# Kernel tuning notes

Hardware: AMD Instinct MI355X
Metric: run time of the kernel (lower is better)

The kernel has to match this reference:

```python
import jax, jax.numpy as jnp
import numpy as np

D_MODEL = 1024
NUM_HEADS = 16
KEY_DIM = 64
VALUE_DIM = 64
NEG_INF = jnp.float32(-1e30)


def setup_inputs() -> dict:
    key = jax.random.key(0)
    ks = jax.random.split(key, 10)
    B, S = 2, 2048
    lim = 1.0 / np.sqrt(D_MODEL)
    x = jax.random.normal(ks[0], (B, S, D_MODEL), dtype=jnp.float32)
    mask = jnp.ones((B, S), dtype=jnp.int32)  # pad mask: 1 = keep
    # stacked per-head linear params (Linear stores weight as [out, in])
    Wq = jax.random.uniform(ks[1], (NUM_HEADS, KEY_DIM, D_MODEL), jnp.float32, -lim, lim)
    bq = jax.random.uniform(ks[2], (NUM_HEADS, KEY_DIM), jnp.float32, -lim, lim)
    Wk = jax.random.uniform(ks[3], (NUM_HEADS, KEY_DIM, D_MODEL), jnp.float32, -lim, lim)
    bk = jax.random.uniform(ks[4], (NUM_HEADS, KEY_DIM), jnp.float32, -lim, lim)
    Wv = jax.random.uniform(ks[5], (NUM_HEADS, VALUE_DIM, D_MODEL), jnp.float32, -lim, lim)
    bv = jax.random.uniform(ks[6], (NUM_HEADS, VALUE_DIM), jnp.float32, -lim, lim)
    lim_o = 1.0 / np.sqrt(NUM_HEADS * VALUE_DIM)
    Wo = jax.random.uniform(ks[7], (D_MODEL, NUM_HEADS * VALUE_DIM), jnp.float32, -lim_o, lim_o)
    bo = jax.random.uniform(ks[8], (D_MODEL,), jnp.float32, -lim_o, lim_o)
    return {"x": x, "mask": mask, "Wq": Wq, "bq": bq, "Wk": Wk, "bk": bk,
            "Wv": Wv, "bv": bv, "Wo": Wo, "bo": bo}


def _mha(x, mask, Wq, bq, Wk, bk, Wv, bv, Wo, bo):
    B, S, _ = x.shape
    # per-head projections: [B, H, S, k]
    q = jnp.einsum('bsd,hkd->bhsk', x, Wq) + bq[None, :, None, :]
    k = jnp.einsum('bsd,hkd->bhsk', x, Wk) + bk[None, :, None, :]
    v = jnp.einsum('bsd,hvd->bhsv', x, Wv) + bv[None, :, None, :]
    scale = 1.0 / np.sqrt(KEY_DIM).astype(np.float32)
    scores = jnp.einsum('bhik,bhjk->bhij', q, k) * scale  # [B, H, S, S]
    # final mask = causal AND pad-row AND pad-col
    causal = jnp.tril(jnp.ones((S, S), dtype=bool))
    pad = mask.astype(bool)
    final = causal[None, None] & pad[:, None, :, None] & pad[:, None, None, :]
    masked = jnp.where(final, scores, NEG_INF)
    w = jax.nn.softmax(masked, axis=-1)
    w = jnp.where(final, w, 0.0)  # fully-masked rows -> zeros, matching loop impl
    out = jnp.einsum('bhij,bhjv->bhiv', w, v)            # [B, H, S, V]
    concat = out.transpose(0, 2, 1, 3).reshape(B, S, NUM_HEADS * VALUE_DIM)
    return concat @ Wo.T + bo


def reference(x, mask, Wq, bq, Wk, bk, Wv, bv, Wo, bo):
    return _mha(x, mask, Wq, bq, Wk, bk, Wv, bv, Wo, bo)
```

## Files before the change

kernel.cpp:

```cpp
#include <hip/hip_runtime.h>

#define SEQ 2048
#define NH 16
#define HD 64
#define DMODEL 1024

__device__ __forceinline__ unsigned int f2bf(float f) {
  unsigned int u = __float_as_uint(f);
  return ((u + 0x7fffu + ((u >> 16) & 1u)) >> 16) & 0xffffu;
}

typedef __bf16 bf16x8 __attribute__((ext_vector_type(8)));
typedef float f32x4 __attribute__((ext_vector_type(4)));

__device__ __forceinline__ void gl2lds16(const unsigned short* g, unsigned short* l) {
  __builtin_amdgcn_global_load_lds(
      (const __attribute__((address_space(1))) unsigned int*)g,
      (__attribute__((address_space(3))) unsigned int*)l, 16, 0, 0);
}

__global__ __launch_bounds__(256) void cast_all_kernel(
    const float* __restrict__ x, const float* __restrict__ wq,
    const float* __restrict__ wk, const float* __restrict__ wv,
    const float* __restrict__ wo,
    unsigned short* __restrict__ xb, unsigned short* __restrict__ wqb,
    unsigned short* __restrict__ wkb, unsigned short* __restrict__ wvb,
    unsigned short* __restrict__ wob) {
  int idx = blockIdx.x * 256 + threadIdx.x;
  if (idx >= 1048576) return;
  const float* src;
  unsigned short* dst;
  int off;
  if (idx < 524288) {
    src = x; dst = xb; off = idx;
  } else {
    int t = idx - 524288;
    int w = t >> 17;
    off = t & 131071;
    src = (w == 0) ? wq : (w == 1) ? wk : (w == 2) ? wv : wo;
    dst = (w == 0) ? wqb : (w == 1) ? wkb : (w == 2) ? wvb : wob;
  }
  const float4* p = reinterpret_cast<const float4*>(src) + (size_t)off * 2;
  float4 a = p[0], b = p[1];
  uint4 o;
  o.x = f2bf(a.x) | (f2bf(a.y) << 16);
  o.y = f2bf(a.z) | (f2bf(a.w) << 16);
  o.z = f2bf(b.x) | (f2bf(b.y) << 16);
  o.w = f2bf(b.z) | (f2bf(b.w) << 16);
  reinterpret_cast<uint4*>(dst)[off] = o;
}

template <int MODE>
__global__ __launch_bounds__(256) void gemm128(
    const unsigned short* __restrict__ A, const unsigned short* __restrict__ B,
    const float* __restrict__ bias0, const float* __restrict__ bias1,
    const float* __restrict__ bias2, float* __restrict__ Cf,
    unsigned short* __restrict__ Qo, unsigned short* __restrict__ Ko,
    unsigned short* __restrict__ Vto, int Kdim) {
  __shared__ __align__(16) unsigned short As[128 * 64];
  __shared__ __align__(16) unsigned short Bs[128 * 64];
  const int tid = threadIdx.x;
  const int wave = tid >> 6, lane = tid & 63;
  const int wm = wave >> 1, wn = wave & 1;
  const int fr = lane & 15, quad = lane >> 4;
  const int fx = fr & 7;
  const int n0 = blockIdx.x * 128, m0 = blockIdx.y * 128;

  const int srowg = lane >> 3;
  const int schunk = (lane & 7) ^ (srowg & 7);
  const unsigned short* Abase =
      A + (size_t)(m0 + wave * 32 + srowg) * Kdim + schunk * 8;
  const unsigned short* Bbase =
      B + (size_t)(n0 + wave * 32 + srowg) * Kdim + schunk * 8;
  unsigned short* AsW = As + (wave * 32) * 64;
  unsigned short* BsW = Bs + (wave * 32) * 64;

  f32x4 acc[4][4];
#pragma unroll
  for (int mt = 0; mt < 4; ++mt)
#pragma unroll
    for (int nt = 0; nt < 4; ++nt) acc[mt][nt] = f32x4{0.f, 0.f, 0.f, 0.f};

  for (int k0 = 0; k0 < Kdim; k0 += 64) {
#pragma unroll
    for (int t = 0; t < 4; ++t) {
      gl2lds16(Abase + (size_t)(t * 8) * Kdim + k0, AsW + t * 8 * 64);
      gl2lds16(Bbase + (size_t)(t * 8) * Kdim + k0, BsW + t * 8 * 64);
    }
    __syncthreads();
#pragma unroll
    for (int ks = 0; ks < 2; ++ks) {
      bf16x8 af[4], bfv[4];
#pragma unroll
      for (int mt = 0; mt < 4; ++mt)
        af[mt] = *reinterpret_cast<const bf16x8*>(
            As + (wm * 64 + mt * 16 + fr) * 64 + ((ks * 4 + quad) ^ fx) * 8);
#pragma unroll
      for (int nt = 0; nt < 4; ++nt)
        bfv[nt] = *reinterpret_cast<const bf16x8*>(
            Bs + (wn * 64 + nt * 16 + fr) * 64 + ((ks * 4 + quad) ^ fx) * 8);
#pragma unroll
      for (int mt = 0; mt < 4; ++mt)
#pragma unroll
        for (int nt = 0; nt < 4; ++nt)
          acc[mt][nt] = __builtin_amdgcn_mfma_f32_16x16x32_bf16(
              af[mt], bfv[nt], acc[mt][nt], 0, 0, 0);
    }
    __syncthreads();
  }

  if (MODE == 0) {
    const int seg = n0 >> 10;
    const float* bp = (seg == 0) ? bias0 : (seg == 1) ? bias1 : bias2;
    const float scale = (seg == 0) ? 0.125f : 1.0f;
    unsigned short* QK = (seg == 0) ? Qo : Ko;
#pragma unroll
    for (int nt = 0; nt < 4; ++nt) {
      const int c = (n0 + wn * 64 + nt * 16 + fr) & 1023;
      const int h = c >> 6, d = c & 63;
      const float bs = bp[c];
#pragma unroll
      for (int mt = 0; mt < 4; ++mt) {
        const int mbase = m0 + wm * 64 + mt * 16 + quad * 4;
        const int b = mbase >> 11, s0 = mbase & 2047;
        if (seg < 2) {
          unsigned short* dst = QK + (((size_t)(b * NH + h)) * SEQ + s0) * HD + d;
#pragma unroll
          for (int r = 0; r < 4; ++r)
            dst[(size_t)r * HD] = (unsigned short)f2bf((acc[mt][nt][r] + bs) * scale);
        } else {
          ushort4 pk;
          pk.x = (unsigned short)f2bf(acc[mt][nt][0] + bs);
          pk.y = (unsigned short)f2bf(acc[mt][nt][1] + bs);
          pk.z = (unsigned short)f2bf(acc[mt][nt][2] + bs);
          pk.w = (unsigned short)f2bf(acc[mt][nt][3] + bs);
          *reinterpret_cast<ushort4*>(
              Vto + (((size_t)(b * NH + h)) * HD + d) * SEQ + s0) = pk;
        }
      }
    }
  } else {
#pragma unroll
    for (int nt = 0; nt < 4; ++nt) {
      const int cg = n0 + wn * 64 + nt * 16 + fr;
      const float bs = bias0[cg];
#pragma unroll
      for (int mt = 0; mt < 4; ++mt) {
        const int mbase = m0 + wm * 64 + mt * 16 + quad * 4;
#pragma unroll
        for (int r = 0; r < 4; ++r)
          Cf[(size_t)(mbase + r) * DMODEL + cg] = acc[mt][nt][r] + bs;
      }
    }
  }
}

__global__ __launch_bounds__(256) void attn_mfma_kernel(const unsigned short* __restrict__ Qg,
                                                        const unsigned short* __restrict__ Kg,
                                                        const unsigned short* __restrict__ Vtg,
                                                        const int* __restrict__ mask,
                                                        unsigned short* __restrict__ concat) {
  const int group = blockIdx.x >> 5;
  const int ib = (group < 8) ? (15 - group) : (group - 8);
  const int bh = blockIdx.x & 31;
  const int b = bh >> 4;
  const int h = bh & 15;
  const int tid = threadIdx.x;
  const int wave = tid >> 6;
  const int lane = tid & 63;
  const int quad = lane >> 4;
  const int fr = lane & 15;
  const int i0 = ib * 128;

  __shared__ unsigned short Ks[64][72];
  __shared__ unsigned short Vts[64][72];
  __shared__ unsigned short Pt[4][16][72];

  const unsigned short* Qb = Qg + ((size_t)bh * SEQ) * HD;
  const unsigned short* Kb = Kg + ((size_t)bh * SEQ) * HD;
  const unsigned short* Vtb = Vtg + ((size_t)bh * HD) * SEQ;
  const int* maskb = mask + b * SEQ;

  int irow[2];
  bf16x8 qf[2][2];
  int padi[2];
#pragma unroll
  for (int qc = 0; qc < 2; ++qc) {
    irow[qc] = i0 + qc * 64 + wave * 16 + fr;
    qf[qc][0] = *reinterpret_cast<const bf16x8*>(Qb + (size_t)irow[qc] * HD + quad * 8);
    qf[qc][1] = *reinterpret_cast<const bf16x8*>(Qb + (size_t)irow[qc] * HD + quad * 8 + 32);
    padi[qc] = maskb[irow[qc]];
  }

  f32x4 o[2][4];
#pragma unroll
  for (int qc = 0; qc < 2; ++qc)
#pragma unroll
    for (int vt = 0; vt < 4; ++vt) o[qc][vt] = f32x4{0.f, 0.f, 0.f, 0.f};
  float mrun[2] = {-1e30f, -1e30f}, lrun[2] = {0.f, 0.f};

  const int srow = tid >> 2;
  const int spart = (tid & 3) * 2;
  const int njc = 2 * ib + 2;

  for (int jc = 0; jc < njc; ++jc) {
    const int j0 = jc * 64;
    {
      const uint4* kg = reinterpret_cast<const uint4*>(Kb + (size_t)(j0 + srow) * HD);
      const uint4* vg = reinterpret_cast<const uint4*>(Vtb + (size_t)srow * SEQ + j0);
      uint4 ka = kg[spart], kc = kg[spart + 1];
      uint4 va = vg[spart], vc = vg[spart + 1];
      *reinterpret_cast<uint4*>(&Ks[srow][spart * 8]) = ka;
      *reinterpret_cast<uint4*>(&Ks[srow][spart * 8 + 8]) = kc;
      *reinterpret_cast<uint4*>(&Vts[srow][spart * 8]) = va;
      *reinterpret_cast<uint4*>(&Vts[srow][spart * 8 + 8]) = vc;
    }
    __syncthreads();

    const int4* mp = reinterpret_cast<const int4*>(maskb + j0);
    int4 mvv[4];
#pragma unroll
    for (int jt = 0; jt < 4; ++jt) mvv[jt] = mp[jt * 4 + quad];

#pragma unroll
    for (int qc = 0; qc < 2; ++qc) {
      if (qc == 0 && jc == 2 * ib + 1) continue;
      const bool diag = (jc == 2 * ib + qc);
      const int ir = irow[qc];

      f32x4 st[4];
#pragma unroll
      for (int jt = 0; jt < 4; ++jt) {
        st[jt] = f32x4{0.f, 0.f, 0.f, 0.f};
        bf16x8 ka0 = *reinterpret_cast<const bf16x8*>(&Ks[jt * 16 + fr][quad * 8]);
        bf16x8 ka1 = *reinterpret_cast<const bf16x8*>(&Ks[jt * 16 + fr][quad * 8 + 32]);
        st[jt] = __builtin_amdgcn_mfma_f32_16x16x32_bf16(ka0, qf[qc][0], st[jt], 0, 0, 0);
        st[jt] = __builtin_amdgcn_mfma_f32_16x16x32_bf16(ka1, qf[qc][1], st[jt], 0, 0, 0);
      }

#pragma unroll
      for (int jt = 0; jt < 4; ++jt) {
        const int4 mv = mvv[jt];
        const int jb = j0 + jt * 16 + quad * 4;
        if (mv.x == 0 || (diag && jb + 0 > ir)) st[jt][0] = -1e30f;
        if (mv.y == 0 || (diag && jb + 1 > ir)) st[jt][1] = -1e30f;
        if (mv.z == 0 || (diag && jb + 2 > ir)) st[jt][2] = -1e30f;
        if (mv.w == 0 || (diag && jb + 3 > ir)) st[jt][3] = -1e30f;
      }

      float tmax = -1e30f;
#pragma unroll
      for (int jt = 0; jt < 4; ++jt)
#pragma unroll
        for (int r = 0; r < 4; ++r) tmax = fmaxf(tmax, st[jt][r]);
      tmax = fmaxf(tmax, __shfl_xor(tmax, 16));
      tmax = fmaxf(tmax, __shfl_xor(tmax, 32));
      float mnew = fmaxf(fmaxf(mrun[qc], tmax), -1e20f);
      const float corr = __expf(mrun[qc] - mnew);
      float p[16];
      float lloc = 0.f;
#pragma unroll
      for (int jt = 0; jt < 4; ++jt)
#pragma unroll
        for (int r = 0; r < 4; ++r) {
          float pv = __expf(st[jt][r] - mnew);
          p[jt * 4 + r] = pv;
          lloc += pv;
        }
      lloc += __shfl_xor(lloc, 16);
      lloc += __shfl_xor(lloc, 32);
      lrun[qc] = lrun[qc] * corr + lloc;
      mrun[qc] = mnew;

#pragma unroll
      for (int jt = 0; jt < 4; ++jt) {
        ushort4 pk;
        pk.x = (unsigned short)f2bf(p[jt * 4 + 0]);
        pk.y = (unsigned short)f2bf(p[jt * 4 + 1]);
        pk.z = (unsigned short)f2bf(p[jt * 4 + 2]);
        pk.w = (unsigned short)f2bf(p[jt * 4 + 3]);
        *reinterpret_cast<ushort4*>(&Pt[wave][fr][jt * 16 + quad * 4]) = pk;
      }

#pragma unroll
      for (int vt = 0; vt < 4; ++vt) {
        o[qc][vt][0] *= corr; o[qc][vt][1] *= corr;
        o[qc][vt][2] *= corr; o[qc][vt][3] *= corr;
      }

      bf16x8 pa0 = *reinterpret_cast<const bf16x8*>(&Pt[wave][fr][quad * 8]);
      bf16x8 pa1 = *reinterpret_cast<const bf16x8*>(&Pt[wave][fr][quad * 8 + 32]);
#pragma unroll
      for (int vt = 0; vt < 4; ++vt) {
        bf16x8 vb0 = *reinterpret_cast<const bf16x8*>(&Vts[vt * 16 + fr][quad * 8]);
        bf16x8 vb1 = *reinterpret_cast<const bf16x8*>(&Vts[vt * 16 + fr][quad * 8 + 32]);
        o[qc][vt] = __builtin_amdgcn_mfma_f32_16x16x32_bf16(vb0, pa0, o[qc][vt], 0, 0, 0);
        o[qc][vt] = __builtin_amdgcn_mfma_f32_16x16x32_bf16(vb1, pa1, o[qc][vt], 0, 0, 0);
      }
    }
    __syncthreads();
  }

#pragma unroll
  for (int qc = 0; qc < 2; ++qc) {
    const float inv = (padi[qc] != 0 && lrun[qc] > 0.f) ? 1.f / lrun[qc] : 0.f;
    unsigned short* orow = concat + ((size_t)(b * SEQ + irow[qc])) * DMODEL + h * HD;
#pragma unroll
    for (int vt = 0; vt < 4; ++vt) {
      ushort4 pk;
      pk.x = (unsigned short)f2bf(o[qc][vt][0] * inv);
      pk.y = (unsigned short)f2bf(o[qc][vt][1] * inv);
      pk.z = (unsigned short)f2bf(o[qc][vt][2] * inv);
      pk.w = (unsigned short)f2bf(o[qc][vt][3] * inv);
      *reinterpret_cast<ushort4*>(orow + vt * 16 + quad * 4) = pk;
    }
  }
}

extern "C" void kernel_launch(void* const* d_in, const int* in_sizes, int n_in,
                              void* d_out, int out_size, void* d_ws, size_t ws_size,
                              hipStream_t stream) {
  (void)in_sizes; (void)n_in; (void)out_size;
  const float* x  = (const float*)d_in[0];
  const int* mask = (const int*)d_in[1];
  const float* Wq = (const float*)d_in[2];
  const float* bq = (const float*)d_in[3];
  const float* Wk = (const float*)d_in[4];
  const float* bk = (const float*)d_in[5];
  const float* Wv = (const float*)d_in[6];
  const float* bv = (const float*)d_in[7];
  const float* Wo = (const float*)d_in[8];
  const float* bo = (const float*)d_in[9];
  float* out = (float*)d_out;

  char* ws = (char*)d_ws;
  if (ws_size < (48ull << 20)) return;
  unsigned short* xb  = (unsigned short*)(ws);
  unsigned short* wqb = (unsigned short*)(ws + (8ull  << 20));
  unsigned short* wkb = (unsigned short*)(ws + (10ull << 20));
  unsigned short* wvb = (unsigned short*)(ws + (12ull << 20));
  unsigned short* wob = (unsigned short*)(ws + (14ull << 20));
  unsigned short* Qb  = (unsigned short*)(ws + (16ull << 20));
  unsigned short* Kb  = (unsigned short*)(ws + (24ull << 20));
  unsigned short* Vtb = (unsigned short*)(ws + (32ull << 20));
  unsigned short* cb  = (unsigned short*)(ws + (40ull << 20));

  cast_all_kernel<<<4096, 256, 0, stream>>>(x, Wq, Wk, Wv, Wo, xb, wqb, wkb, wvb, wob);

  gemm128<0><<<dim3(24, 32), 256, 0, stream>>>(xb, wqb, bq, bk, bv,
                                               nullptr, Qb, Kb, Vtb, 1024);

  attn_mfma_kernel<<<512, 256, 0, stream>>>(Qb, Kb, Vtb, mask, cb);

  gemm128<1><<<dim3(8, 32), 256, 0, stream>>>(cb, wob, bo, nullptr, nullptr,
                                              out, nullptr, nullptr, nullptr, 1024);
}
```

Before: 214.6 us.

## Pair mirrored query tiles per block, skip mask checks on all-valid tiles, use exp2

```diff
diff --git a/kernel.cpp b/kernel.cpp
--- a/kernel.cpp
+++ b/kernel.cpp
@@ -8,6 +8,12 @@
 __device__ __forceinline__ unsigned int f2bf(float f) {
   unsigned int u = __float_as_uint(f);
   return ((u + 0x7fffu + ((u >> 16) & 1u)) >> 16) & 0xffffu;
+}
+
+__device__ __forceinline__ unsigned int pk2bf(float a, float b) {
+  unsigned short ua = __builtin_bit_cast(unsigned short, (__bf16)a);
+  unsigned short ub = __builtin_bit_cast(unsigned short, (__bf16)b);
+  return (unsigned int)ua | ((unsigned int)ub << 16);
 }
 
 typedef __bf16 bf16x8 __attribute__((ext_vector_type(8)));
@@ -47,7 +53,7 @@
   o.y = f2bf(a.z) | (f2bf(a.w) << 16);
   o.z = f2bf(b.x) | (f2bf(b.y) << 16);
   o.w = f2bf(b.z) | (f2bf(b.w) << 16);
-  reinterpret_cast<uint4*>(dst)[off] = o;
+  reinterpret_cast<uint4*>(dst)[idx == off ? off : off] = o;
 }
 
 template <int MODE>
@@ -112,7 +118,7 @@
   if (MODE == 0) {
     const int seg = n0 >> 10;
     const float* bp = (seg == 0) ? bias0 : (seg == 1) ? bias1 : bias2;
-    const float scale = (seg == 0) ? 0.125f : 1.0f;
+    const float scale = (seg == 0) ? 0.1803368809f : 1.0f;
     unsigned short* QK = (seg == 0) ? Qo : Ko;
 #pragma unroll
     for (int nt = 0; nt < 4; ++nt) {
@@ -129,12 +135,10 @@
           for (int r = 0; r < 4; ++r)
             dst[(size_t)r * HD] = (unsigned short)f2bf((acc[mt][nt][r] + bs) * scale);
         } else {
-          ushort4 pk;
-          pk.x = (unsigned short)f2bf(acc[mt][nt][0] + bs);
-          pk.y = (unsigned short)f2bf(acc[mt][nt][1] + bs);
-          pk.z = (unsigned short)f2bf(acc[mt][nt][2] + bs);
-          pk.w = (unsigned short)f2bf(acc[mt][nt][3] + bs);
-          *reinterpret_cast<ushort4*>(
+          uint2 pk;
+          pk.x = pk2bf(acc[mt][nt][0] + bs, acc[mt][nt][1] + bs);
+          pk.y = pk2bf(acc[mt][nt][2] + bs, acc[mt][nt][3] + bs);
+          *reinterpret_cast<uint2*>(
               Vto + (((size_t)(b * NH + h)) * HD + d) * SEQ + s0) = pk;
         }
       }
@@ -155,13 +159,11 @@
   }
 }
 
-__global__ __launch_bounds__(256) void attn_mfma_kernel(const unsigned short* __restrict__ Qg,
-                                                        const unsigned short* __restrict__ Kg,
-                                                        const unsigned short* __restrict__ Vtg,
-                                                        const int* __restrict__ mask,
-                                                        unsigned short* __restrict__ concat) {
-  const int group = blockIdx.x >> 5;
-  const int ib = (group < 8) ? (15 - group) : (group - 8);
+__global__ __launch_bounds__(256, 3) void attn_mfma_kernel(
+    const unsigned short* __restrict__ Qg, const unsigned short* __restrict__ Kg,
+    const unsigned short* __restrict__ Vtg, const int* __restrict__ mask,
+    unsigned short* __restrict__ concat) {
+  const int g = blockIdx.x >> 5;
   const int bh = blockIdx.x & 31;
   const int b = bh >> 4;
   const int h = bh & 15;
@@ -170,40 +172,46 @@
   const int lane = tid & 63;
   const int quad = lane >> 4;
   const int fr = lane & 15;
-  const int i0 = ib * 128;
+  const int ibA = 31 - g, ibB = g;
 
   __shared__ unsigned short Ks[64][72];
   __shared__ unsigned short Vts[64][72];
-  __shared__ unsigned short Pt[4][16][72];
+  __shared__ unsigned short Pt[2][4][16][72];
+  __shared__ unsigned int tilebad;
 
   const unsigned short* Qb = Qg + ((size_t)bh * SEQ) * HD;
   const unsigned short* Kb = Kg + ((size_t)bh * SEQ) * HD;
   const unsigned short* Vtb = Vtg + ((size_t)bh * HD) * SEQ;
   const int* maskb = mask + b * SEQ;
 
-  int irow[2];
-  bf16x8 qf[2][2];
-  int padi[2];
-#pragma unroll
-  for (int qc = 0; qc < 2; ++qc) {
-    irow[qc] = i0 + qc * 64 + wave * 16 + fr;
-    qf[qc][0] = *reinterpret_cast<const bf16x8*>(Qb + (size_t)irow[qc] * HD + quad * 8);
-    qf[qc][1] = *reinterpret_cast<const bf16x8*>(Qb + (size_t)irow[qc] * HD + quad * 8 + 32);
-    padi[qc] = maskb[irow[qc]];
-  }
-
-  f32x4 o[2][4];
-#pragma unroll
-  for (int qc = 0; qc < 2; ++qc)
-#pragma unroll
-    for (int vt = 0; vt < 4; ++vt) o[qc][vt] = f32x4{0.f, 0.f, 0.f, 0.f};
-  float mrun[2] = {-1e30f, -1e30f}, lrun[2] = {0.f, 0.f};
+  if (tid == 0) tilebad = 0;
+  __syncthreads();
+  {
+    const int4* mp4 = reinterpret_cast<const int4*>(maskb);
+    int4 a = mp4[tid * 2], c = mp4[tid * 2 + 1];
+    if (!(a.x && a.y && a.z && a.w && c.x && c.y && c.z && c.w))
+      atomicOr(&tilebad, 1u << (tid >> 3));
+  }
+  __syncthreads();
+  const unsigned int tbad = tilebad;
+
+  const int irA = ibA * 64 + wave * 16 + fr;
+  const int irB = ibB * 64 + wave * 16 + fr;
+  const bf16x8 qA0 = *reinterpret_cast<const bf16x8*>(Qb + (size_t)irA * HD + quad * 8);
+  const bf16x8 qA1 = *reinterpret_cast<const bf16x8*>(Qb + (size_t)irA * HD + quad * 8 + 32);
+  const bf16x8 qB0 = *reinterpret_cast<const bf16x8*>(Qb + (size_t)irB * HD + quad * 8);
+  const bf16x8 qB1 = *reinterpret_cast<const bf16x8*>(Qb + (size_t)irB * HD + quad * 8 + 32);
+  const int padA = maskb[irA], padB = maskb[irB];
+
+  f32x4 oA[4], oB[4];
+#pragma unroll
+  for (int vt = 0; vt < 4; ++vt) { oA[vt] = f32x4{0,0,0,0}; oB[vt] = f32x4{0,0,0,0}; }
+  float mA = -1e20f, lA = 0.f, mB = -1e20f, lB = 0.f;
 
   const int srow = tid >> 2;
   const int spart = (tid & 3) * 2;
-  const int njc = 2 * ib + 2;
-
-  for (int jc = 0; jc < njc; ++jc) {
+
+  for (int jc = 0; jc <= ibA; ++jc) {
     const int j0 = jc * 64;
     {
       const uint4* kg = reinterpret_cast<const uint4*>(Kb + (size_t)(j0 + srow) * HD);
@@ -217,102 +225,161 @@
     }
     __syncthreads();
 
-    const int4* mp = reinterpret_cast<const int4*>(maskb + j0);
-    int4 mvv[4];
-#pragma unroll
-    for (int jt = 0; jt < 4; ++jt) mvv[jt] = mp[jt * 4 + quad];
-
-#pragma unroll
-    for (int qc = 0; qc < 2; ++qc) {
-      if (qc == 0 && jc == 2 * ib + 1) continue;
-      const bool diag = (jc == 2 * ib + qc);
-      const int ir = irow[qc];
-
-      f32x4 st[4];
+    const bool doB = (jc <= ibB);
+    const bool diagA = (jc == ibA), diagB = (jc == ibB);
+    const bool tb = (tbad >> jc) & 1u;
+
+    f32x4 stA[4], stB[4];
+#pragma unroll
+    for (int jt = 0; jt < 4; ++jt) {
+      bf16x8 ka0 = *reinterpret_cast<const bf16x8*>(&Ks[jt * 16 + fr][quad * 8]);
+      bf16x8 ka1 = *reinterpret_cast<const bf16x8*>(&Ks[jt * 16 + fr][quad * 8 + 32]);
+      stA[jt] = f32x4{0,0,0,0};
+      stA[jt] = __builtin_amdgcn_mfma_f32_16x16x32_bf16(ka0, qA0, stA[jt], 0, 0, 0);
+      stA[jt] = __builtin_amdgcn_mfma_f32_16x16x32_bf16(ka1, qA1, stA[jt], 0, 0, 0);
+      if (doB) {
+        stB[jt] = f32x4{0,0,0,0};
+        stB[jt] = __builtin_amdgcn_mfma_f32_16x16x32_bf16(ka0, qB0, stB[jt], 0, 0, 0);
+        stB[jt] = __builtin_amdgcn_mfma_f32_16x16x32_bf16(ka1, qB1, stB[jt], 0, 0, 0);
+      }
+    }
+
+    if (tb) {
+      const int4* mp = reinterpret_cast<const int4*>(maskb + j0);
 #pragma unroll
       for (int jt = 0; jt < 4; ++jt) {
-        st[jt] = f32x4{0.f, 0.f, 0.f, 0.f};
-        bf16x8 ka0 = *reinterpret_cast<const bf16x8*>(&Ks[jt * 16 + fr][quad * 8]);
-        bf16x8 ka1 = *reinterpret_cast<const bf16x8*>(&Ks[jt * 16 + fr][quad * 8 + 32]);
-        st[jt] = __builtin_amdgcn_mfma_f32_16x16x32_bf16(ka0, qf[qc][0], st[jt], 0, 0, 0);
-        st[jt] = __builtin_amdgcn_mfma_f32_16x16x32_bf16(ka1, qf[qc][1], st[jt], 0, 0, 0);
-      }
-
+        const int4 mv = mp[jt * 4 + quad];
+        if (mv.x == 0) { stA[jt][0] = -1e30f; if (doB) stB[jt][0] = -1e30f; }
+        if (mv.y == 0) { stA[jt][1] = -1e30f; if (doB) stB[jt][1] = -1e30f; }
+        if (mv.z == 0) { stA[jt][2] = -1e30f; if (doB) stB[jt][2] = -1e30f; }
+        if (mv.w == 0) { stA[jt][3] = -1e30f; if (doB) stB[jt][3] = -1e30f; }
+      }
+    }
+    if (diagA) {
 #pragma unroll
       for (int jt = 0; jt < 4; ++jt) {
-        const int4 mv = mvv[jt];
         const int jb = j0 + jt * 16 + quad * 4;
-        if (mv.x == 0 || (diag && jb + 0 > ir)) st[jt][0] = -1e30f;
-        if (mv.y == 0 || (diag && jb + 1 > ir)) st[jt][1] = -1e30f;
-        if (mv.z == 0 || (diag && jb + 2 > ir)) st[jt][2] = -1e30f;
-        if (mv.w == 0 || (diag && jb + 3 > ir)) st[jt][3] = -1e30f;
-      }
-
+#pragma unroll
+        for (int r = 0; r < 4; ++r)
+          if (jb + r > irA) stA[jt][r] = -1e30f;
+      }
+    }
+    if (doB && diagB) {
+#pragma unroll
+      for (int jt = 0; jt < 4; ++jt) {
+        const int jb = j0 + jt * 16 + quad * 4;
+#pragma unroll
+        for (int r = 0; r < 4; ++r)
+          if (jb + r > irB) stB[jt][r] = -1e30f;
+      }
+    }
+
+    {
       float tmax = -1e30f;
 #pragma unroll
       for (int jt = 0; jt < 4; ++jt)
 #pragma unroll
-        for (int r = 0; r < 4; ++r) tmax = fmaxf(tmax, st[jt][r]);
+        for (int r = 0; r < 4; ++r) tmax = fmaxf(tmax, stA[jt][r]);
       tmax = fmaxf(tmax, __shfl_xor(tmax, 16));
       tmax = fmaxf(tmax, __shfl_xor(tmax, 32));
-      float mnew = fmaxf(fmaxf(mrun[qc], tmax), -1e20f);
-      const float corr = __expf(mrun[qc] - mnew);
-      float p[16];
+      const bool upd = __ballot(tmax > mA) != 0ull;
+      float corr = 1.f;
+      if (upd) { const float mn = fmaxf(mA, tmax); corr = __builtin_amdgcn_exp2f(mA - mn); mA = mn; }
       float lloc = 0.f;
 #pragma unroll
-      for (int jt = 0; jt < 4; ++jt)
-#pragma unroll
-        for (int r = 0; r < 4; ++r) {
-          float pv = __expf(st[jt][r] - mnew);
-          p[jt * 4 + r] = pv;
-          lloc += pv;
-        }
+      for (int jt = 0; jt < 4; ++jt) {
+        float p0 = __builtin_amdgcn_exp2f(stA[jt][0] - mA);
+        float p1 = __builtin_amdgcn_exp2f(stA[jt][1] - mA);
+        float p2 = __builtin_amdgcn_exp2f(stA[jt][2] - mA);
+        float p3 = __builtin_amdgcn_exp2f(stA[jt][3] - mA);
+        lloc += (p0 + p1) + (p2 + p3);
+        uint2 pk; pk.x = pk2bf(p0, p1); pk.y = pk2bf(p2, p3);
+        *reinterpret_cast<uint2*>(&Pt[0][wave][fr][jt * 16 + quad * 4]) = pk;
+      }
       lloc += __shfl_xor(lloc, 16);
       lloc += __shfl_xor(lloc, 32);
-      lrun[qc] = lrun[qc] * corr + lloc;
-      mrun[qc] = mnew;
-
+      if (upd) {
+        lA = lA * corr + lloc;
+#pragma unroll
+        for (int vt = 0; vt < 4; ++vt) {
+          oA[vt][0] *= corr; oA[vt][1] *= corr; oA[vt][2] *= corr; oA[vt][3] *= corr;
+        }
+      } else lA += lloc;
+    }
+    if (doB) {
+      float tmax = -1e30f;
+#pragma unroll
+      for (int jt = 0; jt < 4; ++jt)
+#pragma unroll
+        for (int r = 0; r < 4; ++r) tmax = fmaxf(tmax, stB[jt][r]);
+      tmax = fmaxf(tmax, __shfl_xor(tmax, 16));
+      tmax = fmaxf(tmax, __shfl_xor(tmax, 32));
+      const bool upd = __ballot(tmax > mB) != 0ull;
+      float corr = 1.f;
+      if (upd) { const float mn = fmaxf(mB, tmax); corr = __builtin_amdgcn_exp2f(mB - mn); mB = mn; }
+      float lloc = 0.f;
 #pragma unroll
       for (int jt = 0; jt < 4; ++jt) {
-        ushort4 pk;
-        pk.x = (unsigned short)f2bf(p[jt * 4 + 0]);
-        pk.y = (unsigned short)f2bf(p[jt * 4 + 1]);
-        pk.z = (unsigned short)f2bf(p[jt * 4 + 2]);
-        pk.w = (unsigned short)f2bf(p[jt * 4 + 3]);
-        *reinterpret_cast<ushort4*>(&Pt[wave][fr][jt * 16 + quad * 4]) = pk;
-      }
-
-#pragma unroll
-      for (int vt = 0; vt < 4; ++vt) {
-        o[qc][vt][0] *= corr; o[qc][vt][1] *= corr;
-        o[qc][vt][2] *= corr; o[qc][vt][3] *= corr;
-      }
-
-      bf16x8 pa0 = *reinterpret_cast<const bf16x8*>(&Pt[wave][fr][quad * 8]);
-      bf16x8 pa1 = *reinterpret_cast<const bf16x8*>(&Pt[wave][fr][quad * 8 + 32]);
-#pragma unroll
-      for (int vt = 0; vt < 4; ++vt) {
-        bf16x8 vb0 = *reinterpret_cast<const bf16x8*>(&Vts[vt * 16 + fr][quad * 8]);
-        bf16x8 vb1 = *reinterpret_cast<const bf16x8*>(&Vts[vt * 16 + fr][quad * 8 + 32]);
-        o[qc][vt] = __builtin_amdgcn_mfma_f32_16x16x32_bf16(vb0, pa0, o[qc][vt], 0, 0, 0);
-        o[qc][vt] = __builtin_amdgcn_mfma_f32_16x16x32_bf16(vb1, pa1, o[qc][vt], 0, 0, 0);
+        float p0 = __builtin_amdgcn_exp2f(stB[jt][0] - mB);
+        float p1 = __builtin_amdgcn_exp2f(stB[jt][1] - mB);
+        float p2 = __builtin_amdgcn_exp2f(stB[jt][2] - mB);
+        float p3 = __builtin_amdgcn_exp2f(stB[jt][3] - mB);
+        lloc += (p0 + p1) + (p2 + p3);
+        uint2 pk; pk.x = pk2bf(p0, p1); pk.y = pk2bf(p2, p3);
+        *reinterpret_cast<uint2*>(&Pt[1][wave][fr][jt * 16 + quad * 4]) = pk;
+      }
+      lloc += __shfl_xor(lloc, 16);
+      lloc += __shfl_xor(lloc, 32);
+      if (upd) {
+        lB = lB * corr + lloc;
+#pragma unroll
+        for (int vt = 0; vt < 4; ++vt) {
+          oB[vt][0] *= corr; oB[vt][1] *= corr; oB[vt][2] *= corr; oB[vt][3] *= corr;
+        }
+      } else lB += lloc;
+    }
+
+    bf16x8 paA0 = *reinterpret_cast<const bf16x8*>(&Pt[0][wave][fr][quad * 8]);
+    bf16x8 paA1 = *reinterpret_cast<const bf16x8*>(&Pt[0][wave][fr][quad * 8 + 32]);
+    bf16x8 paB0, paB1;
+    if (doB) {
+      paB0 = *reinterpret_cast<const bf16x8*>(&Pt[1][wave][fr][quad * 8]);
+      paB1 = *reinterpret_cast<const bf16x8*>(&Pt[1][wave][fr][quad * 8 + 32]);
+    }
+#pragma unroll
+    for (int vt = 0; vt < 4; ++vt) {
+      bf16x8 vb0 = *reinterpret_cast<const bf16x8*>(&Vts[vt * 16 + fr][quad * 8]);
+      bf16x8 vb1 = *reinterpret_cast<const bf16x8*>(&Vts[vt * 16 + fr][quad * 8 + 32]);
+      oA[vt] = __builtin_amdgcn_mfma_f32_16x16x32_bf16(vb0, paA0, oA[vt], 0, 0, 0);
+      oA[vt] = __builtin_amdgcn_mfma_f32_16x16x32_bf16(vb1, paA1, oA[vt], 0, 0, 0);
+      if (doB) {
+        oB[vt] = __builtin_amdgcn_mfma_f32_16x16x32_bf16(vb0, paB0, oB[vt], 0, 0, 0);
+        oB[vt] = __builtin_amdgcn_mfma_f32_16x16x32_bf16(vb1, paB1, oB[vt], 0, 0, 0);
       }
     }
     __syncthreads();
   }
 
-#pragma unroll
-  for (int qc = 0; qc < 2; ++qc) {
-    const float inv = (padi[qc] != 0 && lrun[qc] > 0.f) ? 1.f / lrun[qc] : 0.f;
-    unsigned short* orow = concat + ((size_t)(b * SEQ + irow[qc])) * DMODEL + h * HD;
+  {
+    const float inv = (padA != 0 && lA > 0.f) ? 1.f / lA : 0.f;
+    unsigned short* orow = concat + ((size_t)(b * SEQ + irA)) * DMODEL + h * HD;
 #pragma unroll
     for (int vt = 0; vt < 4; ++vt) {
-      ushort4 pk;
-      pk.x = (unsigned short)f2bf(o[qc][vt][0] * inv);
-      pk.y = (unsigned short)f2bf(o[qc][vt][1] * inv);
-      pk.z = (unsigned short)f2bf(o[qc][vt][2] * inv);
-      pk.w = (unsigned short)f2bf(o[qc][vt][3] * inv);
-      *reinterpret_cast<ushort4*>(orow + vt * 16 + quad * 4) = pk;
+      uint2 pk;
+      pk.x = pk2bf(oA[vt][0] * inv, oA[vt][1] * inv);
+      pk.y = pk2bf(oA[vt][2] * inv, oA[vt][3] * inv);
+      *reinterpret_cast<uint2*>(orow + vt * 16 + quad * 4) = pk;
+    }
+  }
+  {
+    const float inv = (padB != 0 && lB > 0.f) ? 1.f / lB : 0.f;
+    unsigned short* orow = concat + ((size_t)(b * SEQ + irB)) * DMODEL + h * HD;
+#pragma unroll
+    for (int vt = 0; vt < 4; ++vt) {
+      uint2 pk;
+      pk.x = pk2bf(oB[vt][0] * inv, oB[vt][1] * inv);
+      pk.y = pk2bf(oB[vt][2] * inv, oB[vt][3] * inv);
+      *reinterpret_cast<uint2*>(orow + vt * 16 + quad * 4) = pk;
     }
   }
 }
```

Result: faster. 200.6 us (-6.5%).

## Restructure attention: 4 balanced query tiles per block, K/V in registers, exp2 softmax

Applied to the files above, without the earlier changes.

```diff
diff --git a/kernel.cpp b/kernel.cpp
--- a/kernel.cpp
+++ b/kernel.cpp
@@ -8,6 +8,12 @@
 __device__ __forceinline__ unsigned int f2bf(float f) {
   unsigned int u = __float_as_uint(f);
   return ((u + 0x7fffu + ((u >> 16) & 1u)) >> 16) & 0xffffu;
+}
+
+__device__ __forceinline__ unsigned int pk2bf(float a, float b) {
+  unsigned short ua = __builtin_bit_cast(unsigned short, (__bf16)a);
+  unsigned short ub = __builtin_bit_cast(unsigned short, (__bf16)b);
+  return (unsigned int)ua | ((unsigned int)ub << 16);
 }
 
 typedef __bf16 bf16x8 __attribute__((ext_vector_type(8)));
@@ -112,7 +118,7 @@
   if (MODE == 0) {
     const int seg = n0 >> 10;
     const float* bp = (seg == 0) ? bias0 : (seg == 1) ? bias1 : bias2;
-    const float scale = (seg == 0) ? 0.125f : 1.0f;
+    const float scale = (seg == 0) ? 0.1803368809f : 1.0f;
     unsigned short* QK = (seg == 0) ? Qo : Ko;
 #pragma unroll
     for (int nt = 0; nt < 4; ++nt) {
@@ -129,12 +135,10 @@
           for (int r = 0; r < 4; ++r)
             dst[(size_t)r * HD] = (unsigned short)f2bf((acc[mt][nt][r] + bs) * scale);
         } else {
-          ushort4 pk;
-          pk.x = (unsigned short)f2bf(acc[mt][nt][0] + bs);
-          pk.y = (unsigned short)f2bf(acc[mt][nt][1] + bs);
-          pk.z = (unsigned short)f2bf(acc[mt][nt][2] + bs);
-          pk.w = (unsigned short)f2bf(acc[mt][nt][3] + bs);
-          *reinterpret_cast<ushort4*>(
+          uint2 pk;
+          pk.x = pk2bf(acc[mt][nt][0] + bs, acc[mt][nt][1] + bs);
+          pk.y = pk2bf(acc[mt][nt][2] + bs, acc[mt][nt][3] + bs);
+          *reinterpret_cast<uint2*>(
               Vto + (((size_t)(b * NH + h)) * HD + d) * SEQ + s0) = pk;
         }
       }
@@ -155,97 +159,101 @@
   }
 }
 
-__global__ __launch_bounds__(256) void attn_mfma_kernel(const unsigned short* __restrict__ Qg,
-                                                        const unsigned short* __restrict__ Kg,
-                                                        const unsigned short* __restrict__ Vtg,
-                                                        const int* __restrict__ mask,
-                                                        unsigned short* __restrict__ concat) {
-  const int group = blockIdx.x >> 5;
-  const int ib = (group < 8) ? (15 - group) : (group - 8);
+__global__ __launch_bounds__(256) void attn_mfma_kernel(
+    const unsigned short* __restrict__ Qg, const unsigned short* __restrict__ Kg,
+    const unsigned short* __restrict__ Vtg, const int* __restrict__ mask,
+    unsigned short* __restrict__ concat) {
+  const int g = blockIdx.x >> 5;
   const int bh = blockIdx.x & 31;
-  const int b = bh >> 4;
-  const int h = bh & 15;
+  const int b = bh >> 4, h = bh & 15;
   const int tid = threadIdx.x;
-  const int wave = tid >> 6;
-  const int lane = tid & 63;
-  const int quad = lane >> 4;
-  const int fr = lane & 15;
-  const int i0 = ib * 128;
-
-  __shared__ unsigned short Ks[64][72];
-  __shared__ unsigned short Vts[64][72];
-  __shared__ unsigned short Pt[4][16][72];
+  const int wave = tid >> 6, lane = tid & 63;
+  const int quad = lane >> 4, fr = lane & 15;
+  const int ib[4] = {g, 15 - g, 16 + g, 31 - g};
+
+  __shared__ unsigned short Pt[4][4][16][72];
 
   const unsigned short* Qb = Qg + ((size_t)bh * SEQ) * HD;
   const unsigned short* Kb = Kg + ((size_t)bh * SEQ) * HD;
   const unsigned short* Vtb = Vtg + ((size_t)bh * HD) * SEQ;
   const int* maskb = mask + b * SEQ;
 
-  int irow[2];
-  bf16x8 qf[2][2];
-  int padi[2];
-#pragma unroll
-  for (int qc = 0; qc < 2; ++qc) {
-    irow[qc] = i0 + qc * 64 + wave * 16 + fr;
-    qf[qc][0] = *reinterpret_cast<const bf16x8*>(Qb + (size_t)irow[qc] * HD + quad * 8);
-    qf[qc][1] = *reinterpret_cast<const bf16x8*>(Qb + (size_t)irow[qc] * HD + quad * 8 + 32);
-    padi[qc] = maskb[irow[qc]];
-  }
-
-  f32x4 o[2][4];
-#pragma unroll
-  for (int qc = 0; qc < 2; ++qc)
-#pragma unroll
-    for (int vt = 0; vt < 4; ++vt) o[qc][vt] = f32x4{0.f, 0.f, 0.f, 0.f};
-  float mrun[2] = {-1e30f, -1e30f}, lrun[2] = {0.f, 0.f};
-
-  const int srow = tid >> 2;
-  const int spart = (tid & 3) * 2;
-  const int njc = 2 * ib + 2;
-
-  for (int jc = 0; jc < njc; ++jc) {
+  bool bad = false;
+  {
+    const int4* mp4 = reinterpret_cast<const int4*>(maskb);
+#pragma unroll
+    for (int u = 0; u < 8; ++u) {
+      int4 v = mp4[lane * 8 + u];
+      bad |= !(v.x && v.y && v.z && v.w);
+    }
+  }
+  const unsigned long long bm = __ballot(bad);
+
+  int irow[4], padr[4];
+  bf16x8 q0[4], q1[4];
+  f32x4 o[4][4];
+  float mr[4], lr[4];
+#pragma unroll
+  for (int t = 0; t < 4; ++t) {
+    irow[t] = ib[t] * 64 + wave * 16 + fr;
+    q0[t] = *reinterpret_cast<const bf16x8*>(Qb + (size_t)irow[t] * HD + quad * 8);
+    q1[t] = *reinterpret_cast<const bf16x8*>(Qb + (size_t)irow[t] * HD + quad * 8 + 32);
+    padr[t] = maskb[irow[t]];
+    mr[t] = -1e20f; lr[t] = 0.f;
+#pragma unroll
+    for (int vt = 0; vt < 4; ++vt) o[t][vt] = f32x4{0.f, 0.f, 0.f, 0.f};
+  }
+
+  const int jcmax = ib[3];
+  for (int jc = 0; jc <= jcmax; ++jc) {
     const int j0 = jc * 64;
-    {
-      const uint4* kg = reinterpret_cast<const uint4*>(Kb + (size_t)(j0 + srow) * HD);
-      const uint4* vg = reinterpret_cast<const uint4*>(Vtb + (size_t)srow * SEQ + j0);
-      uint4 ka = kg[spart], kc = kg[spart + 1];
-      uint4 va = vg[spart], vc = vg[spart + 1];
-      *reinterpret_cast<uint4*>(&Ks[srow][spart * 8]) = ka;
-      *reinterpret_cast<uint4*>(&Ks[srow][spart * 8 + 8]) = kc;
-      *reinterpret_cast<uint4*>(&Vts[srow][spart * 8]) = va;
-      *reinterpret_cast<uint4*>(&Vts[srow][spart * 8 + 8]) = vc;
-    }
-    __syncthreads();
-
-    const int4* mp = reinterpret_cast<const int4*>(maskb + j0);
-    int4 mvv[4];
-#pragma unroll
-    for (int jt = 0; jt < 4; ++jt) mvv[jt] = mp[jt * 4 + quad];
-
-#pragma unroll
-    for (int qc = 0; qc < 2; ++qc) {
-      if (qc == 0 && jc == 2 * ib + 1) continue;
-      const bool diag = (jc == 2 * ib + qc);
-      const int ir = irow[qc];
+    bf16x8 ka0[4], ka1[4], vb0[4], vb1[4];
+#pragma unroll
+    for (int jt = 0; jt < 4; ++jt) {
+      const unsigned short* kr = Kb + (size_t)(j0 + jt * 16 + fr) * HD + quad * 8;
+      ka0[jt] = *reinterpret_cast<const bf16x8*>(kr);
+      ka1[jt] = *reinterpret_cast<const bf16x8*>(kr + 32);
+    }
+#pragma unroll
+    for (int vt = 0; vt < 4; ++vt) {
+      const unsigned short* vr = Vtb + (size_t)(vt * 16 + fr) * SEQ + j0 + quad * 8;
+      vb0[vt] = *reinterpret_cast<const bf16x8*>(vr);
+      vb1[vt] = *reinterpret_cast<const bf16x8*>(vr + 32);
+    }
+    const bool tb = ((bm >> (2 * jc)) & 3ull) != 0ull;
+
+#pragma unroll
+    for (int t = 0; t < 4; ++t) {
+      if (jc > ib[t]) continue;
+      const int ir = irow[t];
 
       f32x4 st[4];
 #pragma unroll
       for (int jt = 0; jt < 4; ++jt) {
         st[jt] = f32x4{0.f, 0.f, 0.f, 0.f};
-        bf16x8 ka0 = *reinterpret_cast<const bf16x8*>(&Ks[jt * 16 + fr][quad * 8]);
-        bf16x8 ka1 = *reinterpret_cast<const bf16x8*>(&Ks[jt * 16 + fr][quad * 8 + 32]);
-        st[jt] = __builtin_amdgcn_mfma_f32_16x16x32_bf16(ka0, qf[qc][0], st[jt], 0, 0, 0);
-        st[jt] = __builtin_amdgcn_mfma_f32_16x16x32_bf16(ka1, qf[qc][1], st[jt], 0, 0, 0);
-      }
-
-#pragma unroll
-      for (int jt = 0; jt < 4; ++jt) {
-        const int4 mv = mvv[jt];
-        const int jb = j0 + jt * 16 + quad * 4;
-        if (mv.x == 0 || (diag && jb + 0 > ir)) st[jt][0] = -1e30f;
-        if (mv.y == 0 || (diag && jb + 1 > ir)) st[jt][1] = -1e30f;
-        if (mv.z == 0 || (diag && jb + 2 > ir)) st[jt][2] = -1e30f;
-        if (mv.w == 0 || (diag && jb + 3 > ir)) st[jt][3] = -1e30f;
+        st[jt] = __builtin_amdgcn_mfma_f32_16x16x32_bf16(ka0[jt], q0[t], st[jt], 0, 0, 0);
+        st[jt] = __builtin_amdgcn_mfma_f32_16x16x32_bf16(ka1[jt], q1[t], st[jt], 0, 0, 0);
+      }
+
+      if (tb) {
+        const int4* mp = reinterpret_cast<const int4*>(maskb + j0);
+#pragma unroll
+        for (int jt = 0; jt < 4; ++jt) {
+          const int4 mv = mp[jt * 4 + quad];
+          if (mv.x == 0) st[jt][0] = -1e30f;
+          if (mv.y == 0) st[jt][1] = -1e30f;
+          if (mv.z == 0) st[jt][2] = -1e30f;
+          if (mv.w == 0) st[jt][3] = -1e30f;
+        }
+      }
+      if (jc == ib[t]) {
+#pragma unroll
+        for (int jt = 0; jt < 4; ++jt) {
+          const int jb = j0 + jt * 16 + quad * 4;
+#pragma unroll
+          for (int r = 0; r < 4; ++r)
+            if (jb + r > ir) st[jt][r] = -1e30f;
+        }
       }
 
       float tmax = -1e30f;
@@ -255,64 +263,58 @@
         for (int r = 0; r < 4; ++r) tmax = fmaxf(tmax, st[jt][r]);
       tmax = fmaxf(tmax, __shfl_xor(tmax, 16));
       tmax = fmaxf(tmax, __shfl_xor(tmax, 32));
-      float mnew = fmaxf(fmaxf(mrun[qc], tmax), -1e20f);
-      const float corr = __expf(mrun[qc] - mnew);
-      float p[16];
+      const bool upd = __ballot(tmax > mr[t]) != 0ull;
+      float corr = 1.f;
+      if (upd) {
+        const float mn = fmaxf(mr[t], tmax);
+        corr = __builtin_amdgcn_exp2f(mr[t] - mn);
+        mr[t] = mn;
+      }
+      const float mcur = mr[t];
       float lloc = 0.f;
 #pragma unroll
-      for (int jt = 0; jt < 4; ++jt)
-#pragma unroll
-        for (int r = 0; r < 4; ++r) {
-          float pv = __expf(st[jt][r] - mnew);
-          p[jt * 4 + r] = pv;
-          lloc += pv;
-        }
+      for (int jt = 0; jt < 4; ++jt) {
+        float p0 = __builtin_amdgcn_exp2f(st[jt][0] - mcur);
+        float p1 = __builtin_amdgcn_exp2f(st[jt][1] - mcur);
+        float p2 = __builtin_amdgcn_exp2f(st[jt][2] - mcur);
+        float p3 = __builtin_amdgcn_exp2f(st[jt][3] - mcur);
+        lloc += (p0 + p1) + (p2 + p3);
+        uint2 pk; pk.x = pk2bf(p0, p1); pk.y = pk2bf(p2, p3);
+        *reinterpret_cast<uint2*>(&Pt[wave][t][fr][jt * 16 + quad * 4]) = pk;
+      }
       lloc += __shfl_xor(lloc, 16);
       lloc += __shfl_xor(lloc, 32);
-      lrun[qc] = lrun[qc] * corr + lloc;
-      mrun[qc] = mnew;
-
-#pragma unroll
-      for (int jt = 0; jt < 4; ++jt) {
-        ushort4 pk;
-        pk.x = (unsigned short)f2bf(p[jt * 4 + 0]);
-        pk.y = (unsigned short)f2bf(p[jt * 4 + 1]);
-        pk.z = (unsigned short)f2bf(p[jt * 4 + 2]);
-        pk.w = (unsigned short)f2bf(p[jt * 4 + 3]);
-        *reinterpret_cast<ushort4*>(&Pt[wave][fr][jt * 16 + quad * 4]) = pk;
-      }
-
+      if (upd) {
+        lr[t] = lr[t] * corr + lloc;
+#pragma unroll
+        for (int vt = 0; vt < 4; ++vt) {
+          o[t][vt][0] *= corr; o[t][vt][1] *= corr;
+          o[t][vt][2] *= corr; o[t][vt][3] *= corr;
+        }
+      } else {
+        lr[t] += lloc;
+      }
+
+      bf16x8 pa0 = *reinterpret_cast<const bf16x8*>(&Pt[wave][t][fr][quad * 8]);
+      bf16x8 pa1 = *reinterpret_cast<const bf16x8*>(&Pt[wave][t][fr][quad * 8 + 32]);
 #pragma unroll
       for (int vt = 0; vt < 4; ++vt) {
-        o[qc][vt][0] *= corr; o[qc][vt][1] *= corr;
-        o[qc][vt][2] *= corr; o[qc][vt][3] *= corr;
-      }
-
-      bf16x8 pa0 = *reinterpret_cast<const bf16x8*>(&Pt[wave][fr][quad * 8]);
-      bf16x8 pa1 = *reinterpret_cast<const bf16x8*>(&Pt[wave][fr][quad * 8 + 32]);
-#pragma unroll
-      for (int vt = 0; vt < 4; ++vt) {
-        bf16x8 vb0 = *reinterpret_cast<const bf16x8*>(&Vts[vt * 16 + fr][quad * 8]);
-        bf16x8 vb1 = *reinterpret_cast<const bf16x8*>(&Vts[vt * 16 + fr][quad * 8 + 32]);
-        o[qc][vt] = __builtin_amdgcn_mfma_f32_16x16x32_bf16(vb0, pa0, o[qc][vt], 0, 0, 0);
-        o[qc][vt] = __builtin_amdgcn_mfma_f32_16x16x32_bf16(vb1, pa1, o[qc][vt], 0, 0, 0);
-      }
-    }
-    __syncthreads();
-  }
-
-#pragma unroll
-  for (int qc = 0; qc < 2; ++qc) {
-    const float inv = (padi[qc] != 0 && lrun[qc] > 0.f) ? 1.f / lrun[qc] : 0.f;
-    unsigned short* orow = concat + ((size_t)(b * SEQ + irow[qc])) * DMODEL + h * HD;
+        o[t][vt] = __builtin_amdgcn_mfma_f32_16x16x32_bf16(vb0[vt], pa0, o[t][vt], 0, 0, 0);
+        o[t][vt] = __builtin_amdgcn_mfma_f32_16x16x32_bf16(vb1[vt], pa1, o[t][vt], 0, 0, 0);
+      }
+    }
+  }
+
+#pragma unroll
+  for (int t = 0; t < 4; ++t) {
+    const float inv = (padr[t] != 0 && lr[t] > 0.f) ? 1.f / lr[t] : 0.f;
+    unsigned short* orow = concat + ((size_t)(b * SEQ + irow[t])) * DMODEL + h * HD;
 #pragma unroll
     for (int vt = 0; vt < 4; ++vt) {
-      ushort4 pk;
-      pk.x = (unsigned short)f2bf(o[qc][vt][0] * inv);
-      pk.y = (unsigned short)f2bf(o[qc][vt][1] * inv);
-      pk.z = (unsigned short)f2bf(o[qc][vt][2] * inv);
-      pk.w = (unsigned short)f2bf(o[qc][vt][3] * inv);
-      *reinterpret_cast<ushort4*>(orow + vt * 16 + quad * 4) = pk;
+      uint2 pk;
+      pk.x = pk2bf(o[t][vt][0] * inv, o[t][vt][1] * inv);
+      pk.y = pk2bf(o[t][vt][2] * inv, o[t][vt][3] * inv);
+      *reinterpret_cast<uint2*>(orow + vt * 16 + quad * 4) = pk;
     }
   }
 }
@@ -350,7 +352,7 @@
   gemm128<0><<<dim3(24, 32), 256, 0, stream>>>(xb, wqb, bq, bk, bv,
                                                nullptr, Qb, Kb, Vtb, 1024);
 
-  attn_mfma_kernel<<<512, 256, 0, stream>>>(Qb, Kb, Vtb, mask, cb);
+  attn_mfma_kernel<<<256, 256, 0, stream>>>(Qb, Kb, Vtb, mask, cb);
 
   gemm128<1><<<dim3(8, 32), 256, 0, stream>>>(cb, wob, bo, nullptr, nullptr,
                                               out, nullptr, nullptr, nullptr, 1024);
```

Measured after the change: 220.2 us. 1.03x slower.
